# Optimization experiments

Hardware: AMD Instinct MI355X
Metric: run time of the kernel (lower is better)

The kernel has to match this reference:

```python
import jax, jax.numpy as jnp
import numpy as np

D_MODEL = 2048
N_HEADS = 16
D_HEAD = D_MODEL // N_HEADS
ROPE_THETA = 10000.0


def setup_inputs() -> dict:
    key = jax.random.key(0)
    ks = jax.random.split(key, 3)
    B, T = 4, 2048
    x = jax.random.normal(ks[0], (B, T, D_MODEL), dtype=jnp.float32)
    # torch Linear weights stored transposed to (in, out) so y = x @ w + b
    w_qkv = jax.random.normal(ks[1], (D_MODEL, 3 * D_MODEL), dtype=jnp.float32) * (1.0 / np.sqrt(D_MODEL))
    b_qkv = jnp.zeros((3 * D_MODEL,), dtype=jnp.float32)
    w_out = jax.random.normal(ks[2], (D_MODEL, D_MODEL), dtype=jnp.float32) * (1.0 / np.sqrt(D_MODEL))
    b_out = jnp.zeros((D_MODEL,), dtype=jnp.float32)
    return {"x": x, "w_qkv": w_qkv, "b_qkv": b_qkv, "w_out": w_out, "b_out": b_out}


def _apply_rope(t, position_offset=0):
    # t: (B, H, T, d_head). Standard rotate-half RoPE.
    T = t.shape[2]
    inv_freq = 1.0 / (ROPE_THETA ** (jnp.arange(0, D_HEAD, 2, dtype=jnp.float32) / D_HEAD))
    pos = jnp.arange(T, dtype=jnp.float32) + position_offset
    freqs = jnp.einsum("t,f->tf", pos, inv_freq)            # (T, d_head/2)
    emb = jnp.concatenate([freqs, freqs], axis=-1)           # (T, d_head)
    cos = jnp.cos(emb)[None, None, :, :]
    sin = jnp.sin(emb)[None, None, :, :]
    t1, t2 = jnp.split(t, 2, axis=-1)
    rot = jnp.concatenate([-t2, t1], axis=-1)
    return t * cos + rot * sin


def reference(x, w_qkv, b_qkv, w_out, b_out):
    B, T, D = x.shape
    scale = 1.0 / np.sqrt(D_HEAD)
    qkv = x @ w_qkv + b_qkv                                   # (B, T, 3D)
    q, k, v = jnp.split(qkv, 3, axis=-1)
    def to_heads(a):
        return a.reshape(B, T, N_HEADS, D_HEAD).transpose(0, 2, 1, 3)  # (B,H,T,dh)
    q, k, v = to_heads(q), to_heads(k), to_heads(v)
    q = _apply_rope(q)
    k = _apply_rope(k)
    scores = jnp.einsum("bhqd,bhkd->bhqk", q, k) * scale      # (B,H,T,T)
    causal = jnp.triu(jnp.full((T, T), -jnp.inf, dtype=scores.dtype), k=1)
    scores = scores + causal
    attn = jax.nn.softmax(scores, axis=-1)                    # dropout p=0 (eval)
    ctx = jnp.einsum("bhqk,bhkd->bhqd", attn, v)
    ctx = ctx.transpose(0, 2, 1, 3).reshape(B, T, D)
    out = ctx @ w_out + b_out
    return out
```

## Files before the change

### kernel.cpp

```cpp
#include <hip/hip_runtime.h>

#define D_MODEL 2048
#define NHEADS 16
#define DHEAD 128
#define TSEQ 2048
#define BATCH 4
#define MROWS (BATCH*TSEQ)
#define NQKV (3*D_MODEL)
#define BH (BATCH*NHEADS)

typedef __attribute__((ext_vector_type(4))) float f32x4;
typedef __attribute__((ext_vector_type(8))) __bf16 bf16x8;
typedef __attribute__((ext_vector_type(4))) unsigned int u32x4;

__device__ inline unsigned short f2bf(float f) {
  union { float f; unsigned u; } v; v.f = f;
  unsigned r = (v.u + 0x7fffu + ((v.u >> 16) & 1u)) >> 16;
  return (unsigned short)r;
}
__device__ inline unsigned short f2bf_t(float f) {
  union { float f; unsigned u; } v; v.f = f;
  return (unsigned short)(v.u >> 16);
}
__device__ inline float bf2f(unsigned short h) {
  union { unsigned u; float f; } v; v.u = ((unsigned)h) << 16; return v.f;
}

__device__ inline void gl_lds16(const unsigned short* g, unsigned short* l) {
  __builtin_amdgcn_global_load_lds(
      (const __attribute__((address_space(1))) unsigned int*)g,
      (__attribute__((address_space(3))) unsigned int*)l, 16, 0, 0);
}

#define CFENCE asm volatile("" ::: "memory")
#define BAR do { CFENCE; __builtin_amdgcn_s_barrier(); CFENCE; } while (0)
#define VM(n) asm volatile("s_waitcnt vmcnt(" #n ")" ::: "memory")
#define LGKM0 asm volatile("s_waitcnt lgkmcnt(0)" ::: "memory")

__global__ __launch_bounds__(256) void cvt_bf16(const float* __restrict__ in,
                                                unsigned short* __restrict__ out, int n) {
  int i = (blockIdx.x * 256 + threadIdx.x) * 8;
  if (i >= n) return;
  float4 a = *(const float4*)(in + i);
  float4 b = *(const float4*)(in + i + 4);
  union { unsigned short s[8]; u32x4 v; } r;
  r.s[0] = f2bf(a.x); r.s[1] = f2bf(a.y); r.s[2] = f2bf(a.z); r.s[3] = f2bf(a.w);
  r.s[4] = f2bf(b.x); r.s[5] = f2bf(b.y); r.s[6] = f2bf(b.z); r.s[7] = f2bf(b.w);
  *(u32x4*)(out + i) = r.v;
}

__global__ __launch_bounds__(256) void transw(const float* __restrict__ w,
                                              unsigned short* __restrict__ wt, int K, int N) {
  __shared__ float tile[32][33];
  int n0 = blockIdx.x * 32, k0 = blockIdx.y * 32;
  int x = threadIdx.x & 31, y = threadIdx.x >> 5;
  #pragma unroll
  for (int j = 0; j < 4; ++j)
    tile[y + j * 8][x] = w[(size_t)(k0 + y + j * 8) * N + n0 + x];
  __syncthreads();
  #pragma unroll
  for (int j = 0; j < 4; ++j)
    wt[(size_t)(n0 + y + j * 8) * K + k0 + x] = f2bf(tile[x][y + j * 8]);
}

__global__ void rope_table(float2* __restrict__ tab) {
  int t = blockIdx.x, f = threadIdx.x;
  float inv = __expf(-0.14391156831212787f * (float)f);
  float ang = (float)t * inv;
  tab[t * 64 + f] = make_float2(cosf(ang), sinf(ang));
}

__global__ __launch_bounds__(256) void rope_apply(unsigned short* __restrict__ X,
                                                  const float2* __restrict__ tab,
                                                  float osc) {
  int row = blockIdx.x * 4 + (threadIdx.x >> 6);
  int f = threadIdx.x & 63;
  int t = row & (TSEQ - 1);
  unsigned short* p = X + (size_t)row * DHEAD;
  float2 cs = tab[t * 64 + f];
  float x1 = bf2f(p[f]), x2 = bf2f(p[f + 64]);
  p[f]      = f2bf((x1 * cs.x - x2 * cs.y) * osc);
  p[f + 64] = f2bf((x2 * cs.x + x1 * cs.y) * osc);
}

template<int MH, int NH>
__device__ inline void mmaq(f32x4 (&acc)[8][4], const bf16x8 (&av)[4][2], const bf16x8 (&bv)[2][2]) {
  #pragma unroll
  for (int m = 0; m < 4; ++m)
    #pragma unroll
    for (int n = 0; n < 2; ++n)
      #pragma unroll
      for (int kk = 0; kk < 2; ++kk)
        acc[MH * 4 + m][NH * 2 + n] =
            __builtin_amdgcn_mfma_f32_16x16x32_bf16(av[m][kk], bv[n][kk],
                                                    acc[MH * 4 + m][NH * 2 + n], 0, 0, 0);
}

__device__ inline void rdhalf(bf16x8 (&dst)[4][2], const unsigned short* base,
                              int rbase, int l15, int l16) {
  #pragma unroll
  for (int m = 0; m < 4; ++m)
    #pragma unroll
    for (int kk = 0; kk < 2; ++kk)
      dst[m][kk] = *(const bf16x8*)&base[(rbase + m * 16 + l15) * 64 +
                                         ((((kk << 2) | l16) ^ (l15 & 7)) << 3)];
}

__device__ inline void rdhalf2(bf16x8 (&dst)[2][2], const unsigned short* base,
                               int rbase, int l15, int l16) {
  #pragma unroll
  for (int n = 0; n < 2; ++n)
    #pragma unroll
    for (int kk = 0; kk < 2; ++kk)
      dst[n][kk] = *(const bf16x8*)&base[(rbase + n * 16 + l15) * 64 +
                                         ((((kk << 2) | l16) ^ (l15 & 7)) << 3)];
}

template<int MODE>
__global__ __launch_bounds__(512, 2) void gemm_bt(
    const unsigned short* __restrict__ A,
    const unsigned short* __restrict__ Bt,
    const float* __restrict__ bias,
    int M, int N, int K,
    unsigned short* __restrict__ Qb,
    unsigned short* __restrict__ Kb,
    unsigned short* __restrict__ VTb,
    float* __restrict__ outF)
{
  __shared__ unsigned short A_lds[2][2][128 * 64];
  __shared__ unsigned short B_lds[2][2][128 * 64];
  int tid = threadIdx.x;
  int wid = tid >> 6, lane = tid & 63;
  int wm = wid >> 2, wn = wid & 3;
  int l15 = lane & 15, l16 = lane >> 4;
  int row0 = blockIdx.y * 256, col0 = blockIdx.x * 256;

  const unsigned short* Ab = A + (size_t)row0 * K;
  const unsigned short* Bb = Bt + (size_t)col0 * K;
  int r8 = tid >> 3;
  int koff = (((tid & 7) ^ (r8 & 7)) << 3);

#define STAGE_A(par, h, tc) do { \
    const unsigned short* g_ = Ab + (size_t)((h) * 128 + r8) * K + (tc) + koff; \
    gl_lds16(g_, &A_lds[par][h][tid * 8]); \
    gl_lds16(g_ + (size_t)64 * K, &A_lds[par][h][(512 + tid) * 8]); } while (0)
#define STAGE_B(par, h, tc) do { \
    const unsigned short* g_ = Bb + (size_t)((h) * 128 + r8) * K + (tc) + koff; \
    gl_lds16(g_, &B_lds[par][h][tid * 8]); \
    gl_lds16(g_ + (size_t)64 * K, &B_lds[par][h][(512 + tid) * 8]); } while (0)

  f32x4 acc[8][4] = {};
  bf16x8 a0[4][2], a1[4][2], b0[2][2], b1[2][2];
  int NT = K >> 6;

  STAGE_A(0, 0, 0); STAGE_B(0, 0, 0); STAGE_A(0, 1, 0); STAGE_B(0, 1, 0);
  VM(4); BAR;

  for (int kt = 0; kt < NT - 1; ++kt) {
    int par = kt & 1, parn = par ^ 1;
    int kn = (kt + 1) << 6;
    rdhalf(a0, &A_lds[par][0][0], wm * 64, l15, l16);
    rdhalf2(b0, &B_lds[par][0][0], wn * 32, l15, l16);
    STAGE_A(parn, 0, kn); STAGE_B(parn, 0, kn);
    VM(6); BAR; LGKM0;
    __builtin_amdgcn_s_setprio(1);
    mmaq<0, 0>(acc, a0, b0);
    __builtin_amdgcn_s_setprio(0);
    rdhalf(a1, &A_lds[par][1][0], wm * 64, l15, l16);
    STAGE_A(parn, 1, kn);
    VM(6); BAR; LGKM0;
    __builtin_amdgcn_s_setprio(1);
    mmaq<1, 0>(acc, a1, b0);
    __builtin_amdgcn_s_setprio(0);
    rdhalf2(b1, &B_lds[par][1][0], wn * 32, l15, l16);
    STAGE_B(parn, 1, kn);
    __builtin_amdgcn_s_setprio(1);
    mmaq<0, 1>(acc, a0, b1);
    __builtin_amdgcn_s_setprio(0);
    VM(4); BAR;
    __builtin_amdgcn_s_setprio(1);
    mmaq<1, 1>(acc, a1, b1);
    __builtin_amdgcn_s_setprio(0);
  }

  {
    int par = (NT - 1) & 1;
    rdhalf(a0, &A_lds[par][0][0], wm * 64, l15, l16);
    rdhalf2(b0, &B_lds[par][0][0], wn * 32, l15, l16);
    VM(2); BAR; LGKM0;
    __builtin_amdgcn_s_setprio(1);
    mmaq<0, 0>(acc, a0, b0);
    __builtin_amdgcn_s_setprio(0);
    rdhalf(a1, &A_lds[par][1][0], wm * 64, l15, l16);
    VM(0); BAR;
    rdhalf2(b1, &B_lds[par][1][0], wn * 32, l15, l16);
    __builtin_amdgcn_s_setprio(1);
    mmaq<1, 0>(acc, a1, b0);
    mmaq<0, 1>(acc, a0, b1);
    mmaq<1, 1>(acc, a1, b1);
    __builtin_amdgcn_s_setprio(0);
  }

  #pragma unroll
  for (int am = 0; am < 8; ++am) {
    int mh = am >> 2, m = am & 3;
    #pragma unroll
    for (int an = 0; an < 4; ++an) {
      int nh = an >> 1, n = an & 1;
      int col = col0 + nh * 128 + wn * 32 + n * 16 + l15;
      float bs = bias[col];
      #pragma unroll
      for (int r = 0; r < 4; ++r) {
        int row = row0 + mh * 128 + wm * 64 + m * 16 + l16 * 4 + r;
        float val = acc[am][an][r] + bs;
        if (MODE == 0) {
          int which = col >> 11;
          int rem = col & 2047;
          int h = rem >> 7, dh = rem & 127;
          int b = row >> 11, t = row & 2047;
          int bh = b * NHEADS + h;
          if (which == 0)      Qb[((size_t)bh * TSEQ + t) * DHEAD + dh] = f2bf(val);
          else if (which == 1) Kb[((size_t)bh * TSEQ + t) * DHEAD + dh] = f2bf(val);
          else                 VTb[((size_t)bh * DHEAD + dh) * TSEQ + t] = f2bf(val);
        } else {
          outF[(size_t)row * N + col] = val;
        }
      }
    }
  }
#undef STAGE_A
#undef STAGE_B
}

__global__ __launch_bounds__(256, 2) void attn_fwd(
    const unsigned short* __restrict__ Qb,
    const unsigned short* __restrict__ Kb,
    const unsigned short* __restrict__ VTb,
    unsigned short* __restrict__ ctx)
{
  __shared__ unsigned short Ksm[2][64 * 128];
  __shared__ unsigned short Vsm[2][128 * 64];
  __shared__ unsigned short Psm[4][32 * 64];
  int bid = blockIdx.x;
  int bh = bid & 63, pr = bid >> 6;
  int hi = 15 - pr, lo = pr;
  int tid = threadIdx.x, wid = tid >> 6, lane = tid & 63;
  int l15 = lane & 15, l16 = lane >> 4;
  const unsigned short* Kh = Kb + (size_t)bh * TSEQ * DHEAD;
  const unsigned short* Vh = VTb + (size_t)bh * DHEAD * TSEQ;
  unsigned short* P = &Psm[wid][0];
  int swzl = (l15 & 7) << 4;

  int krow = tid >> 4;
  int kcol = (((tid & 15) << 4) ^ ((krow & 7) << 4)) >> 1;
  int vrow = tid >> 3;
  int vcol = (((tid & 7) << 4) ^ ((vrow & 7) << 4)) >> 1;
  int ldsl = tid * 8;

  int ck[4];
  #pragma unroll
  for (int kk = 0; kk < 4; ++kk) ck[kk] = ((kk * 64 + l16 * 16) ^ swzl) >> 1;

  bf16x8 qf[2][4];
  f32x4 accO[2][8];
  float mrow[2][4], lrow[2][4];

  int qbase = hi * 128 + wid * 32;
  #pragma unroll
  for (int m = 0; m < 2; ++m) {
    #pragma unroll
    for (int n = 0; n < 8; ++n) accO[m][n] = (f32x4)0.f;
    #pragma unroll
    for (int r = 0; r < 4; ++r) { mrow[m][r] = -1e30f; lrow[m][r] = 0.f; }
    #pragma unroll
    for (int kk = 0; kk < 4; ++kk)
      qf[m][kk] = *(const bf16x8*)&Qb[((size_t)bh * TSEQ + qbase + m * 16 + l15) * DHEAD
                                      + kk * 32 + l16 * 8];
  }

  int nt0 = 2 * hi + 2;
  int ntt = nt0 + 2 * lo + 2;

  {
    const unsigned short* kg = Kh + krow * DHEAD + kcol;
    const unsigned short* vg = Vh + (size_t)vrow * TSEQ + vcol;
    #pragma unroll
    for (int ps = 0; ps < 4; ++ps) {
      gl_lds16(kg + ps * 16 * DHEAD, &Ksm[0][ldsl + ps * 2048]);
      gl_lds16(vg + (size_t)ps * 32 * TSEQ, &Vsm[0][ldsl + ps * 2048]);
    }
  }
  __syncthreads();

  for (int it = 0; it < ntt; ++it) {
    int buf = it & 1;
    int kv0 = ((it >= nt0) ? (it - nt0) : it) * 64;

    if (it + 1 < ntt) {
      int n2 = it + 1;
      int kv2 = ((n2 >= nt0) ? (n2 - nt0) : n2) * 64;
      const unsigned short* kg = Kh + (size_t)(kv2 + krow) * DHEAD + kcol;
      const unsigned short* vg = Vh + (size_t)vrow * TSEQ + kv2 + vcol;
      #pragma unroll
      for (int ps = 0; ps < 4; ++ps) {
        gl_lds16(kg + ps * 16 * DHEAD, &Ksm[buf ^ 1][ldsl + ps * 2048]);
        gl_lds16(vg + (size_t)ps * 32 * TSEQ, &Vsm[buf ^ 1][ldsl + ps * 2048]);
      }
    }

    if (kv0 <= qbase + 31) {
      const unsigned short* Kt = Ksm[buf];
      const unsigned short* Vt = Vsm[buf];

      f32x4 S[2][4] = {};
      #pragma unroll
      for (int n = 0; n < 4; ++n) {
        bf16x8 kf[4];
        #pragma unroll
        for (int kk = 0; kk < 4; ++kk)
          kf[kk] = *(const bf16x8*)&Kt[(n * 16 + l15) * DHEAD + ck[kk]];
        #pragma unroll
        for (int m = 0; m < 2; ++m)
          #pragma unroll
          for (int kk = 0; kk < 4; ++kk)
            S[m][n] = __builtin_amdgcn_mfma_f32_16x16x32_bf16(qf[m][kk], kf[kk], S[m][n], 0, 0, 0);
      }

      bool masked = (kv0 + 63 > qbase);
      float lmax[2][4];
      float grow = -1e30f;
      #pragma unroll
      for (int m = 0; m < 2; ++m) {
        #pragma unroll
        for (int r = 0; r < 4; ++r) {
          if (masked) {
            int qg = qbase + m * 16 + l16 * 4 + r;
            if (kv0 + l15      > qg) S[m][0][r] = -1e30f;
            if (kv0 + 16 + l15 > qg) S[m][1][r] = -1e30f;
            if (kv0 + 32 + l15 > qg) S[m][2][r] = -1e30f;
            if (kv0 + 48 + l15 > qg) S[m][3][r] = -1e30f;
          }
          float v = fmaxf(fmaxf(S[m][0][r], S[m][1][r]), fmaxf(S[m][2][r], S[m][3][r]));
          lmax[m][r] = v;
          grow = fmaxf(grow, v - mrow[m][r]);
        }
      }

      if (__any(grow > 8.f)) {
        #pragma unroll
        for (int m = 0; m < 2; ++m)
          #pragma unroll
          for (int r = 0; r < 4; ++r) {
            float v = lmax[m][r];
            #pragma unroll
            for (int off = 1; off < 16; off <<= 1) v = fmaxf(v, __shfl_xor(v, off));
            float mnew = fmaxf(mrow[m][r], v);
            float alpha = exp2f(mrow[m][r] - mnew);
            mrow[m][r] = mnew;
            lrow[m][r] *= alpha;
            #pragma unroll
            for (int n = 0; n < 8; ++n) accO[m][n][r] *= alpha;
          }
      }

      #pragma unroll
      for (int m = 0; m < 2; ++m) {
        #pragma unroll
        for (int r = 0; r < 4; ++r) {
          float mr = mrow[m][r];
          float p0 = exp2f(S[m][0][r] - mr), p1 = exp2f(S[m][1][r] - mr);
          float p2 = exp2f(S[m][2][r] - mr), p3 = exp2f(S[m][3][r] - mr);
          lrow[m][r] += (p0 + p1) + (p2 + p3);
          int qr = m * 16 + l16 * 4 + r;
          int ws = (qr & 7) << 4;
          P[qr * 64 + ((((l15 << 1))      ^ ws) >> 1)] = f2bf_t(p0);
          P[qr * 64 + (((32 + (l15 << 1)) ^ ws) >> 1)] = f2bf_t(p1);
          P[qr * 64 + (((64 + (l15 << 1)) ^ ws) >> 1)] = f2bf_t(p2);
          P[qr * 64 + (((96 + (l15 << 1)) ^ ws) >> 1)] = f2bf_t(p3);
        }
      }

      bf16x8 pf[2][2];
      #pragma unroll
      for (int m = 0; m < 2; ++m)
        #pragma unroll
        for (int kk = 0; kk < 2; ++kk)
          pf[m][kk] = *(const bf16x8*)&P[(m * 16 + l15) * 64 + ck[kk]];
      #pragma unroll
      for (int n = 0; n < 8; ++n) {
        bf16x8 vf[2];
        #pragma unroll
        for (int kk = 0; kk < 2; ++kk)
          vf[kk] = *(const bf16x8*)&Vt[(n * 16 + l15) * 64 + ck[kk]];
        #pragma unroll
        for (int m = 0; m < 2; ++m)
          #pragma unroll
          for (int kk = 0; kk < 2; ++kk)
            accO[m][n] = __builtin_amdgcn_mfma_f32_16x16x32_bf16(pf[m][kk], vf[kk], accO[m][n], 0, 0, 0);
      }
    }

    if (it == nt0 - 1) {
      int b = bh >> 4, h = bh & 15;
      #pragma unroll
      for (int m = 0; m < 2; ++m)
        #pragma unroll
        for (int r = 0; r < 4; ++r) {
          float ls = lrow[m][r];
          #pragma unroll
          for (int off = 1; off < 16; off <<= 1) ls += __shfl_xor(ls, off);
          float inv = 1.0f / ls;
          int t = qbase + m * 16 + l16 * 4 + r;
          size_t base = ((size_t)b * TSEQ + t) * D_MODEL + h * DHEAD;
          #pragma unroll
          for (int n = 0; n < 8; ++n)
            ctx[base + n * 16 + l15] = f2bf(accO[m][n][r] * inv);
        }
      qbase = lo * 128 + wid * 32;
      #pragma unroll
      for (int m = 0; m < 2; ++m) {
        #pragma unroll
        for (int n = 0; n < 8; ++n) accO[m][n] = (f32x4)0.f;
        #pragma unroll
        for (int r = 0; r < 4; ++r) { mrow[m][r] = -1e30f; lrow[m][r] = 0.f; }
        #pragma unroll
        for (int kk = 0; kk < 4; ++kk)
          qf[m][kk] = *(const bf16x8*)&Qb[((size_t)bh * TSEQ + qbase + m * 16 + l15) * DHEAD
                                          + kk * 32 + l16 * 8];
      }
    }

    __syncthreads();
  }

  {
    int b = bh >> 4, h = bh & 15;
    #pragma unroll
    for (int m = 0; m < 2; ++m)
      #pragma unroll
      for (int r = 0; r < 4; ++r) {
        float ls = lrow[m][r];
        #pragma unroll
        for (int off = 1; off < 16; off <<= 1) ls += __shfl_xor(ls, off);
        float inv = 1.0f / ls;
        int t = qbase + m * 16 + l16 * 4 + r;
        size_t base = ((size_t)b * TSEQ + t) * D_MODEL + h * DHEAD;
        #pragma unroll
        for (int n = 0; n < 8; ++n)
          ctx[base + n * 16 + l15] = f2bf(accO[m][n][r] * inv);
      }
  }
}

extern "C" void kernel_launch(void* const* d_in, const int* in_sizes, int n_in,
                              void* d_out, int out_size, void* d_ws, size_t ws_size,
                              hipStream_t stream)
{
  const float* x     = (const float*)d_in[0];
  const float* w_qkv = (const float*)d_in[1];
  const float* b_qkv = (const float*)d_in[2];
  const float* w_out = (const float*)d_in[3];
  const float* b_out = (const float*)d_in[4];
  float* out = (float*)d_out;

  unsigned short* xb    = (unsigned short*)d_ws;
  unsigned short* wqkvT = xb    + (size_t)MROWS * D_MODEL;
  unsigned short* woutT = wqkvT + (size_t)NQKV * D_MODEL;
  unsigned short* Qb    = woutT + (size_t)D_MODEL * D_MODEL;
  unsigned short* Kb    = Qb    + (size_t)BH * TSEQ * DHEAD;
  unsigned short* VTb   = Kb    + (size_t)BH * TSEQ * DHEAD;
  float2* tab = (float2*)(VTb + (size_t)BH * TSEQ * DHEAD);

  const float SCALE_Q = 0.08838834764831845f * 1.4426950408889634f;

  cvt_bf16<<<MROWS * D_MODEL / 2048, 256, 0, stream>>>(x, xb, MROWS * D_MODEL);
  transw<<<dim3(NQKV / 32, D_MODEL / 32), 256, 0, stream>>>(w_qkv, wqkvT, D_MODEL, NQKV);
  transw<<<dim3(D_MODEL / 32, D_MODEL / 32), 256, 0, stream>>>(w_out, woutT, D_MODEL, D_MODEL);
  rope_table<<<TSEQ, 64, 0, stream>>>(tab);
  gemm_bt<0><<<dim3(NQKV / 256, MROWS / 256), 512, 0, stream>>>(
      xb, wqkvT, b_qkv, MROWS, NQKV, D_MODEL, Qb, Kb, VTb, nullptr);
  rope_apply<<<BH * TSEQ / 4, 256, 0, stream>>>(Qb, tab, SCALE_Q);
  rope_apply<<<BH * TSEQ / 4, 256, 0, stream>>>(Kb, tab, 1.0f);
  attn_fwd<<<dim3(512), 256, 0, stream>>>(Qb, Kb, VTb, xb);
  gemm_bt<1><<<dim3(D_MODEL / 256, MROWS / 256), 512, 0, stream>>>(
      xb, woutT, b_out, MROWS, D_MODEL, D_MODEL, nullptr, nullptr, nullptr, out);
}
```

Before: 466.6 us.

## Fuse RoPE and Q scaling into QKV GEMM epilogue via LDS staging

Removes the two standalone rope_apply kernels and applies RoPE (plus the Q softmax scale) inside the QKV GEMM epilogue. Q/K output tiles are staged through the reused LDS buffers in fp32, so each thread can read the partner element 64 columns away, rotate it, and write bf16 directly. This saves an extra read-modify-write pass over Q and K in global memory and two kernel launches, at the cost of extra barriers and LDS traffic in the epilogue. It also drops one bf16 rounding before the rotation.

```diff
diff --git a/kernel.cpp b/kernel.cpp
--- a/kernel.cpp
+++ b/kernel.cpp
@@ -70,19 +70,6 @@
   tab[t * 64 + f] = make_float2(cosf(ang), sinf(ang));
 }
 
-__global__ __launch_bounds__(256) void rope_apply(unsigned short* __restrict__ X,
-                                                  const float2* __restrict__ tab,
-                                                  float osc) {
-  int row = blockIdx.x * 4 + (threadIdx.x >> 6);
-  int f = threadIdx.x & 63;
-  int t = row & (TSEQ - 1);
-  unsigned short* p = X + (size_t)row * DHEAD;
-  float2 cs = tab[t * 64 + f];
-  float x1 = bf2f(p[f]), x2 = bf2f(p[f + 64]);
-  p[f]      = f2bf((x1 * cs.x - x2 * cs.y) * osc);
-  p[f + 64] = f2bf((x2 * cs.x + x1 * cs.y) * osc);
-}
-
 template<int MH, int NH>
 __device__ inline void mmaq(f32x4 (&acc)[8][4], const bf16x8 (&av)[4][2], const bf16x8 (&bv)[2][2]) {
   #pragma unroll
@@ -125,10 +112,10 @@
     unsigned short* __restrict__ Qb,
     unsigned short* __restrict__ Kb,
     unsigned short* __restrict__ VTb,
-    float* __restrict__ outF)
+    float* __restrict__ outF,
+    const float2* __restrict__ tab)
 {
-  __shared__ unsigned short A_lds[2][2][128 * 64];
-  __shared__ unsigned short B_lds[2][2][128 * 64];
+  __shared__ unsigned short LDSU[2][2][2][128 * 64];
   int tid = threadIdx.x;
   int wid = tid >> 6, lane = tid & 63;
   int wm = wid >> 2, wn = wid & 3;
@@ -142,12 +129,12 @@
 
 #define STAGE_A(par, h, tc) do { \
     const unsigned short* g_ = Ab + (size_t)((h) * 128 + r8) * K + (tc) + koff; \
-    gl_lds16(g_, &A_lds[par][h][tid * 8]); \
-    gl_lds16(g_ + (size_t)64 * K, &A_lds[par][h][(512 + tid) * 8]); } while (0)
+    gl_lds16(g_, &LDSU[0][par][h][tid * 8]); \
+    gl_lds16(g_ + (size_t)64 * K, &LDSU[0][par][h][(512 + tid) * 8]); } while (0)
 #define STAGE_B(par, h, tc) do { \
     const unsigned short* g_ = Bb + (size_t)((h) * 128 + r8) * K + (tc) + koff; \
-    gl_lds16(g_, &B_lds[par][h][tid * 8]); \
-    gl_lds16(g_ + (size_t)64 * K, &B_lds[par][h][(512 + tid) * 8]); } while (0)
+    gl_lds16(g_, &LDSU[1][par][h][tid * 8]); \
+    gl_lds16(g_ + (size_t)64 * K, &LDSU[1][par][h][(512 + tid) * 8]); } while (0)
 
   f32x4 acc[8][4] = {};
   bf16x8 a0[4][2], a1[4][2], b0[2][2], b1[2][2];
@@ -159,20 +146,20 @@
   for (int kt = 0; kt < NT - 1; ++kt) {
     int par = kt & 1, parn = par ^ 1;
     int kn = (kt + 1) << 6;
-    rdhalf(a0, &A_lds[par][0][0], wm * 64, l15, l16);
-    rdhalf2(b0, &B_lds[par][0][0], wn * 32, l15, l16);
+    rdhalf(a0, &LDSU[0][par][0][0], wm * 64, l15, l16);
+    rdhalf2(b0, &LDSU[1][par][0][0], wn * 32, l15, l16);
     STAGE_A(parn, 0, kn); STAGE_B(parn, 0, kn);
     VM(6); BAR; LGKM0;
     __builtin_amdgcn_s_setprio(1);
     mmaq<0, 0>(acc, a0, b0);
     __builtin_amdgcn_s_setprio(0);
-    rdhalf(a1, &A_lds[par][1][0], wm * 64, l15, l16);
+    rdhalf(a1, &LDSU[0][par][1][0], wm * 64, l15, l16);
     STAGE_A(parn, 1, kn);
     VM(6); BAR; LGKM0;
     __builtin_amdgcn_s_setprio(1);
     mmaq<1, 0>(acc, a1, b0);
     __builtin_amdgcn_s_setprio(0);
-    rdhalf2(b1, &B_lds[par][1][0], wn * 32, l15, l16);
+    rdhalf2(b1, &LDSU[1][par][1][0], wn * 32, l15, l16);
     STAGE_B(parn, 1, kn);
     __builtin_amdgcn_s_setprio(1);
     mmaq<0, 1>(acc, a0, b1);
@@ -185,15 +172,15 @@
 
   {
     int par = (NT - 1) & 1;
-    rdhalf(a0, &A_lds[par][0][0], wm * 64, l15, l16);
-    rdhalf2(b0, &B_lds[par][0][0], wn * 32, l15, l16);
+    rdhalf(a0, &LDSU[0][par][0][0], wm * 64, l15, l16);
+    rdhalf2(b0, &LDSU[1][par][0][0], wn * 32, l15, l16);
     VM(2); BAR; LGKM0;
     __builtin_amdgcn_s_setprio(1);
     mmaq<0, 0>(acc, a0, b0);
     __builtin_amdgcn_s_setprio(0);
-    rdhalf(a1, &A_lds[par][1][0], wm * 64, l15, l16);
+    rdhalf(a1, &LDSU[0][par][1][0], wm * 64, l15, l16);
     VM(0); BAR;
-    rdhalf2(b1, &B_lds[par][1][0], wn * 32, l15, l16);
+    rdhalf2(b1, &LDSU[1][par][1][0], wn * 32, l15, l16);
     __builtin_amdgcn_s_setprio(1);
     mmaq<1, 0>(acc, a1, b0);
     mmaq<0, 1>(acc, a0, b1);
@@ -201,29 +188,81 @@
     __builtin_amdgcn_s_setprio(0);
   }
 
-  #pragma unroll
-  for (int am = 0; am < 8; ++am) {
-    int mh = am >> 2, m = am & 3;
-    #pragma unroll
-    for (int an = 0; an < 4; ++an) {
-      int nh = an >> 1, n = an & 1;
-      int col = col0 + nh * 128 + wn * 32 + n * 16 + l15;
-      float bs = bias[col];
-      #pragma unroll
-      for (int r = 0; r < 4; ++r) {
-        int row = row0 + mh * 128 + wm * 64 + m * 16 + l16 * 4 + r;
-        float val = acc[am][an][r] + bs;
-        if (MODE == 0) {
-          int which = col >> 11;
+  if (MODE == 0 && (col0 >> 8) < 16) {
+    const float SCQ = 0.08838834764831845f * 1.4426950408889634f;
+    bool isQ = (col0 >> 8) < 8;
+    float* Lf = (float*)&LDSU[0][0][0][0];
+    BAR;
+    #pragma unroll
+    for (int c = 0; c < 2; ++c) {
+      #pragma unroll
+      for (int m = 0; m < 4; ++m) {
+        #pragma unroll
+        for (int an = 0; an < 4; ++an) {
+          int nh = an >> 1, n = an & 1;
+          int col_l = nh * 128 + wn * 32 + n * 16 + l15;
+          float bs = bias[col0 + col_l];
+          #pragma unroll
+          for (int r = 0; r < 4; ++r) {
+            int row_l = wm * 64 + m * 16 + l16 * 4 + r;
+            int swz = ((row_l >> 2) & 3) << 3;
+            Lf[row_l * 256 + (col_l ^ swz)] = acc[c * 4 + m][an][r] + bs;
+          }
+        }
+      }
+      BAR;
+      #pragma unroll
+      for (int m = 0; m < 4; ++m) {
+        #pragma unroll
+        for (int an = 0; an < 4; ++an) {
+          int nh = an >> 1, n = an & 1;
+          int col_l = nh * 128 + wn * 32 + n * 16 + l15;
+          int col = col0 + col_l;
           int rem = col & 2047;
           int h = rem >> 7, dh = rem & 127;
-          int b = row >> 11, t = row & 2047;
-          int bh = b * NHEADS + h;
-          if (which == 0)      Qb[((size_t)bh * TSEQ + t) * DHEAD + dh] = f2bf(val);
-          else if (which == 1) Kb[((size_t)bh * TSEQ + t) * DHEAD + dh] = f2bf(val);
-          else                 VTb[((size_t)bh * DHEAD + dh) * TSEQ + t] = f2bf(val);
-        } else {
-          outF[(size_t)row * N + col] = val;
+          #pragma unroll
+          for (int r = 0; r < 4; ++r) {
+            int row_l = wm * 64 + m * 16 + l16 * 4 + r;
+            int swz = ((row_l >> 2) & 3) << 3;
+            float v1 = Lf[row_l * 256 + (col_l ^ swz)];
+            float v2 = Lf[row_l * 256 + ((col_l ^ 64) ^ swz)];
+            int row = row0 + c * 128 + row_l;
+            int t = row & 2047;
+            float2 cs = tab[t * 64 + (dh & 63)];
+            float o = (dh & 64) ? (v1 * cs.x + v2 * cs.y)
+                                : (v1 * cs.x - v2 * cs.y);
+            if (isQ) o *= SCQ;
+            int b = row >> 11;
+            int bh = b * NHEADS + h;
+            if (isQ) Qb[((size_t)bh * TSEQ + t) * DHEAD + dh] = f2bf(o);
+            else     Kb[((size_t)bh * TSEQ + t) * DHEAD + dh] = f2bf(o);
+          }
+        }
+      }
+      BAR;
+    }
+  } else {
+    #pragma unroll
+    for (int am = 0; am < 8; ++am) {
+      int mh = am >> 2, m = am & 3;
+      #pragma unroll
+      for (int an = 0; an < 4; ++an) {
+        int nh = an >> 1, n = an & 1;
+        int col = col0 + nh * 128 + wn * 32 + n * 16 + l15;
+        float bs = bias[col];
+        #pragma unroll
+        for (int r = 0; r < 4; ++r) {
+          int row = row0 + mh * 128 + wm * 64 + m * 16 + l16 * 4 + r;
+          float val = acc[am][an][r] + bs;
+          if (MODE == 0) {
+            int rem = col & 2047;
+            int h = rem >> 7, dh = rem & 127;
+            int b = row >> 11, t = row & 2047;
+            int bh = b * NHEADS + h;
+            VTb[((size_t)bh * DHEAD + dh) * TSEQ + t] = f2bf(val);
+          } else {
+            outF[(size_t)row * N + col] = val;
+          }
         }
       }
     }
@@ -471,17 +510,13 @@
   unsigned short* VTb   = Kb    + (size_t)BH * TSEQ * DHEAD;
   float2* tab = (float2*)(VTb + (size_t)BH * TSEQ * DHEAD);
 
-  const float SCALE_Q = 0.08838834764831845f * 1.4426950408889634f;
-
   cvt_bf16<<<MROWS * D_MODEL / 2048, 256, 0, stream>>>(x, xb, MROWS * D_MODEL);
   transw<<<dim3(NQKV / 32, D_MODEL / 32), 256, 0, stream>>>(w_qkv, wqkvT, D_MODEL, NQKV);
   transw<<<dim3(D_MODEL / 32, D_MODEL / 32), 256, 0, stream>>>(w_out, woutT, D_MODEL, D_MODEL);
   rope_table<<<TSEQ, 64, 0, stream>>>(tab);
   gemm_bt<0><<<dim3(NQKV / 256, MROWS / 256), 512, 0, stream>>>(
-      xb, wqkvT, b_qkv, MROWS, NQKV, D_MODEL, Qb, Kb, VTb, nullptr);
-  rope_apply<<<BH * TSEQ / 4, 256, 0, stream>>>(Qb, tab, SCALE_Q);
-  rope_apply<<<BH * TSEQ / 4, 256, 0, stream>>>(Kb, tab, 1.0f);
+      xb, wqkvT, b_qkv, MROWS, NQKV, D_MODEL, Qb, Kb, VTb, nullptr, tab);
   attn_fwd<<<dim3(512), 256, 0, stream>>>(Qb, Kb, VTb, xb);
   gemm_bt<1><<<dim3(D_MODEL / 256, MROWS / 256), 512, 0, stream>>>(
-      xb, woutT, b_out, MROWS, D_MODEL, D_MODEL, nullptr, nullptr, nullptr, out);
-}
+      xb, woutT, b_out, MROWS, D_MODEL, D_MODEL, nullptr, nullptr, nullptr, out, nullptr);
+}
```

After: 447.7 us. 4.0% less time.
